# Optimization experiments

Hardware: AMD Instinct MI355X
Metric: run time of the kernel (lower is better)

## Reference

```python
import jax, jax.numpy as jnp
import numpy as np

N_NODES = 50000
N_EDGES = 800000
D_NODE = 128
D_EDGE = 64
N_GC = 2
H = 256
N_GRAPHS = 512


def setup_inputs() -> dict:
    key = jax.random.key(0)
    ks = jax.random.split(key, 32)
    s = 0.05
    inp = {
        'x': jax.random.normal(ks[0], (N_NODES, D_NODE), jnp.float32),
        'edge_index': jax.random.randint(ks[1], (2, N_EDGES), 0, N_NODES, jnp.int64 if jax.config.jax_enable_x64 else jnp.int32),
        'edge_attr': jax.random.normal(ks[2], (N_EDGES, D_EDGE), jnp.float32),
        'batch': jnp.sort(jax.random.randint(ks[3], (N_NODES,), 0, N_GRAPHS)),
    }
    zin = 2 * D_NODE + D_EDGE  # 320
    inp['conv_Wf'] = jax.random.normal(ks[4], (N_GC, D_NODE, zin), jnp.float32) * s
    inp['conv_bf'] = jnp.zeros((N_GC, D_NODE), jnp.float32)
    inp['conv_Ws'] = jax.random.normal(ks[5], (N_GC, D_NODE, zin), jnp.float32) * s
    inp['conv_bs'] = jnp.zeros((N_GC, D_NODE), jnp.float32)
    # mlp_1: Linear(128->256), ReLU, Linear(256->256), ReLU, proj Linear(256->128)
    inp['mlp1_W0'] = jax.random.normal(ks[6], (H, D_NODE), jnp.float32) * s
    inp['mlp1_b0'] = jnp.zeros((H,), jnp.float32)
    inp['mlp1_W1'] = jax.random.normal(ks[7], (H, H), jnp.float32) * s
    inp['mlp1_b1'] = jnp.zeros((H,), jnp.float32)
    inp['mlp1_Wp'] = jax.random.normal(ks[8], (D_NODE, H), jnp.float32) * s
    inp['mlp1_bp'] = jnp.zeros((D_NODE,), jnp.float32)
    # mlp_2: same structure
    inp['mlp2_W0'] = jax.random.normal(ks[9], (H, D_NODE), jnp.float32) * s
    inp['mlp2_b0'] = jnp.zeros((H,), jnp.float32)
    inp['mlp2_W1'] = jax.random.normal(ks[10], (H, H), jnp.float32) * s
    inp['mlp2_b1'] = jnp.zeros((H,), jnp.float32)
    inp['mlp2_Wp'] = jax.random.normal(ks[11], (D_NODE, H), jnp.float32) * s
    inp['mlp2_bp'] = jnp.zeros((D_NODE,), jnp.float32)
    inp['out_W'] = jax.random.normal(ks[12], (1, D_NODE), jnp.float32) * s
    inp['out_b'] = jnp.zeros((1,), jnp.float32)
    return inp


def _mlp(x, W0, b0, W1, b1, Wp, bp):
    h = jax.nn.relu(x @ W0.T + b0)
    h = jax.nn.relu(h @ W1.T + b1)
    return h @ Wp.T + bp


def _cgconv(x, src, dst, edge_attr, Wf, bf, Ws, bs):
    # z = [x_i (target), x_j (source), edge_attr]  -> [E, 2D+De]
    z = jnp.concatenate([x[dst], x[src], edge_attr], axis=-1)
    msg = jax.nn.sigmoid(z @ Wf.T + bf) * jax.nn.softplus(z @ Ws.T + bs)
    aggr = jax.ops.segment_sum(msg, dst, num_segments=x.shape[0])
    return x + aggr  # CGConv residual


def reference(x, edge_index, edge_attr, batch,
              conv_Wf, conv_bf, conv_Ws, conv_bs,
              mlp1_W0, mlp1_b0, mlp1_W1, mlp1_b1, mlp1_Wp, mlp1_bp,
              mlp2_W0, mlp2_b0, mlp2_W1, mlp2_b1, mlp2_Wp, mlp2_bp,
              out_W, out_b):
    src, dst = edge_index[0], edge_index[1]
    out = x
    for l in range(N_GC):
        out = _cgconv(out, src, dst, edge_attr, conv_Wf[l], conv_bf[l], conv_Ws[l], conv_bs[l])
    out = out + _mlp(out, mlp1_W0, mlp1_b0, mlp1_W1, mlp1_b1, mlp1_Wp, mlp1_bp)
    out = jax.ops.segment_sum(out, batch, num_segments=N_GRAPHS)  # global_add_pool
    out = out + _mlp(out, mlp2_W0, mlp2_b0, mlp2_W1, mlp2_b1, mlp2_Wp, mlp2_bp)
    out = out @ out_W.T + out_b  # [n_graphs, 1]
    return out
```

## Files before the change

### kernel.cpp

```cpp
#include <hip/hip_runtime.h>
#include <stdint.h>

#define NN 50000
#define NE 800000
#define DN 128
#define DE 64
#define NG 512
#define HD 256
#define LDA 72
#define SPK_S 132

typedef unsigned short ushort_t;
typedef __attribute__((ext_vector_type(8))) short short8;
typedef __attribute__((ext_vector_type(4))) float floatx4;

__device__ __forceinline__ float bflo(unsigned u){ unsigned v=u<<16; float f; __builtin_memcpy(&f,&v,4); return f; }
__device__ __forceinline__ float bfhi(unsigned u){ unsigned v=u&0xffff0000u; float f; __builtin_memcpy(&f,&v,4); return f; }
__device__ __forceinline__ ushort_t f2bf(float f){ unsigned u; __builtin_memcpy(&u,&f,4); u += 0x7FFFu + ((u>>16)&1u); return (ushort_t)(u>>16); }
__device__ __forceinline__ unsigned cvtpk(float a, float b){
#if __has_builtin(__builtin_amdgcn_cvt_pk_bf16_f32)
  auto r = __builtin_amdgcn_cvt_pk_bf16_f32(a,b);
  unsigned u; __builtin_memcpy(&u,&r,4); return u;
#else
  return (unsigned)f2bf(a) | ((unsigned)f2bf(b)<<16);
#endif
}

__device__ __forceinline__ float actv(float fv, float sv){
  const float L2E = 1.44269504f, LN2 = 0.69314718f;
  float ef  = __builtin_amdgcn_exp2f(-L2E*fv);
  float sig = __builtin_amdgcn_rcpf(1.f+ef);
  float t   = __builtin_amdgcn_exp2f(-L2E*fabsf(sv));
  float sp  = fmaxf(sv,0.f) + LN2*__builtin_amdgcn_logf(1.f+t);
  return sig*sp;
}

__global__ void k_prep(const float* __restrict__ Wf, const float* __restrict__ Ws,
                       const float* __restrict__ W0, const float* __restrict__ W1, const float* __restrict__ Wp,
                       const float* __restrict__ cbf, const float* __restrict__ cbs,
                       ushort_t* Wnode, ushort_t* Wedge, ushort_t* W0b, ushort_t* W1b, ushort_t* Wpb,
                       float* bias512){
  int i = blockIdx.x*256 + threadIdx.x;
  if(i < 131072){
    int l = i >> 16, r = i & 65535;
    int n = r >> 7, k = r & 127;
    const float* W = (n<256)? Wf : Ws;
    int nn = n & 127;
    int koff = ((n>>7)&1) ? 128+k : k;
    Wnode[i] = f2bf(W[(size_t)l*128*320 + (size_t)nn*320 + koff]);
  } else if(i < 163840){
    int j = i - 131072;
    int l = j >> 14, r = j & 16383;
    int n = r >> 6, k = r & 63;
    const float* W = (n<128)? Wf : Ws;
    int nn = n & 127;
    Wedge[j] = f2bf(W[(size_t)l*128*320 + (size_t)nn*320 + 256 + k]);
  } else if(i < 196608){
    int j = i - 163840; W0b[j] = f2bf(W0[j]);
  } else if(i < 262144){
    int j = i - 196608; W1b[j] = f2bf(W1[j]);
  } else if(i < 294912){
    int j = i - 262144; Wpb[j] = f2bf(Wp[j]);
  } else if(i < 295936){
    int j = i - 294912;
    int l = j >> 9, c = j & 511;
    float v = 0.f;
    if(c < 128) v = cbf[l*128 + c];
    else if(c >= 256 && c < 384) v = cbs[l*128 + (c-256)];
    bias512[j] = v;
  }
}

__global__ void k_init_x(const float* x, float* xcur, ushort_t* xb){
  int i = blockIdx.x*256 + threadIdx.x;
  if(i < NN*DN){ float v = x[i]; xcur[i]=v; xb[i]=f2bf(v); }
}

__global__ void k_zero_u32(unsigned* p, int n){
  int i = blockIdx.x*256 + threadIdx.x;
  if(i<n) p[i]=0u;
}

__global__ void k_hist(const int* dst, int* deg){
  int i = blockIdx.x*256 + threadIdx.x;
  if(i<NE) atomicAdd(&deg[dst[i]], 1);
}

__global__ void k_blocksum(const int* deg, int* bsum, int n){
  __shared__ int s[256];
  int t = threadIdx.x, i = blockIdx.x*256 + t;
  s[t] = (i<n)? deg[i] : 0;
  __syncthreads();
  for(int o=128;o>0;o>>=1){ if(t<o) s[t]+=s[t+o]; __syncthreads(); }
  if(t==0) bsum[blockIdx.x]=s[0];
}

__global__ void k_scan_bsum(int* bsum, int nb, int* offs, int nnodes){
  __shared__ int s[2][256];
  int t = threadIdx.x;
  int v = (t<nb)? bsum[t] : 0;
  s[0][t]=v; __syncthreads();
  int cur=0;
  for(int o=1;o<256;o<<=1){
    int nx=cur^1;
    s[nx][t] = s[cur][t] + ((t>=o)? s[cur][t-o] : 0);
    cur=nx; __syncthreads();
  }
  if(t<nb) bsum[t] = s[cur][t] - v;
  if(t==255) offs[nnodes] = s[cur][255];
}

__global__ void k_scanscatter(const int* deg, const int* bsum, int* offs, int* cursor, int n){
  __shared__ int s[2][256];
  int t=threadIdx.x, i=blockIdx.x*256+t;
  int v=(i<n)? deg[i] : 0;
  s[0][t]=v; __syncthreads();
  int cur=0;
  for(int o=1;o<256;o<<=1){
    int nx=cur^1;
    s[nx][t] = s[cur][t] + ((t>=o)? s[cur][t-o] : 0);
    cur=nx; __syncthreads();
  }
  if(i<n){ int ex = s[cur][t]-v + bsum[blockIdx.x]; offs[i]=ex; cursor[i]=ex; }
}

__global__ void k_scatter(const int* dst, int* cursor, int* csr_pos){
  int i = blockIdx.x*256 + threadIdx.x;
  if(i<NE){ int pos = atomicAdd(&cursor[dst[i]], 1); csr_pos[i]=pos; }
}

__global__ __launch_bounds__(256) void k_gemm(const ushort_t* __restrict__ Ain, const ushort_t* __restrict__ Wg,
      int M, int N, int K, const float* __restrict__ bias, int mode,
      ushort_t* __restrict__ outb, float* __restrict__ outf, const float* __restrict__ addf){
  __shared__ __align__(16) ushort_t As[64*LDA];
  __shared__ __align__(16) ushort_t Bs[64*LDA];
  int tid = threadIdx.x;
  int m0 = blockIdx.x*64, n0 = blockIdx.y*64;
  int w = tid>>6, lane = tid&63, row16 = lane&15, quad = lane>>4;
  floatx4 acc[4];
  #pragma unroll
  for(int t=0;t<4;t++) acc[t]=(floatx4)(0.f);
  int nk = K>>6;
  for(int kc=0; kc<nk; kc++){
    #pragma unroll
    for(int i=0;i<2;i++){
      int lin = tid + i*256;
      int row = lin>>3, c8 = (lin&7)*8;
      uint4 va;
      int gm = m0+row;
      if(gm < M) va = *(const uint4*)&Ain[(size_t)gm*K + kc*64 + c8];
      else va = make_uint4(0,0,0,0);
      *(uint4*)&As[row*LDA + c8] = va;
      uint4 vb = *(const uint4*)&Wg[(size_t)(n0+row)*K + kc*64 + c8];
      *(uint4*)&Bs[row*LDA + c8] = vb;
    }
    __syncthreads();
    #pragma unroll
    for(int ks=0;ks<2;ks++){
      short8 a = *(const short8*)&As[(w*16+row16)*LDA + ks*32 + quad*8];
      #pragma unroll
      for(int t=0;t<4;t++){
        short8 b = *(const short8*)&Bs[(t*16+row16)*LDA + ks*32 + quad*8];
        acc[t] = __builtin_amdgcn_mfma_f32_16x16x32_bf16(a,b,acc[t],0,0,0);
      }
    }
    __syncthreads();
  }
  #pragma unroll
  for(int t=0;t<4;t++){
    int nn = n0 + t*16 + row16;
    #pragma unroll
    for(int r=0;r<4;r++){
      int m = m0 + w*16 + quad*4 + r;
      if(m>=M) continue;
      float v = acc[t][r];
      if(bias) v += bias[nn];
      if(mode==1){ v = v>0.f? v:0.f; outb[(size_t)m*N+nn]=f2bf(v); }
      else if(mode==2){ v += addf[(size_t)m*N+nn]; outf[(size_t)m*N+nn]=v; }
      else { outb[(size_t)m*N+nn]=f2bf(v); }
    }
  }
}

__global__ __launch_bounds__(256) void k_edge_msg(const float* __restrict__ ea,
      const int* __restrict__ src_g, const int* __restrict__ dst_g,
      const int* __restrict__ csr_pos,
      const ushort_t* __restrict__ Wedge, const ushort_t* __restrict__ Atab,
      ushort_t* __restrict__ msg){
  __shared__ __align__(16) char smem[46848];
  ushort_t* We  = (ushort_t*)smem;
  unsigned* spk = (unsigned*)smem;
  ushort_t* el  = (ushort_t*)(smem + 36864);
  int*      dl  = (int*)(smem + 46080);
  int*      sl  = (int*)(smem + 46336);
  int*      cp  = (int*)(smem + 46592);

  int tid = threadIdx.x;
  int e0 = blockIdx.x*64;
  {
    const uint4* s = (const uint4*)Wedge;
    #pragma unroll
    for(int i=0;i<8;i++){
      int idx = tid + i*256;
      int row = idx>>3, col = (idx&7)*8;
      *(uint4*)&We[row*LDA + col] = s[idx];
    }
  }
  {
    int row = tid>>2, c0 = (tid&3)*16;
    const float4* p = (const float4*)&ea[(size_t)(e0+row)*64 + c0];
    float4 f0=p[0], f1=p[1], f2=p[2], f3=p[3];
    uint4 q0, q1;
    q0.x=cvtpk(f0.x,f0.y); q0.y=cvtpk(f0.z,f0.w); q0.z=cvtpk(f1.x,f1.y); q0.w=cvtpk(f1.z,f1.w);
    q1.x=cvtpk(f2.x,f2.y); q1.y=cvtpk(f2.z,f2.w); q1.z=cvtpk(f3.x,f3.y); q1.w=cvtpk(f3.z,f3.w);
    *(uint4*)&el[row*LDA + c0] = q0;
    *(uint4*)&el[row*LDA + c0 + 8] = q1;
  }
  if(tid<64){ dl[tid]=dst_g[e0+tid]; sl[tid]=src_g[e0+tid]; }
  else if(tid>=64 && tid<128){ cp[tid-64]=csr_pos[e0+tid-64]; }
  __syncthreads();

  int w = tid>>6, lane = tid&63, row16 = lane&15, quad = lane>>4;
  floatx4 acc[16];
  #pragma unroll
  for(int t=0;t<16;t++) acc[t]=(floatx4)(0.f);
  #pragma unroll
  for(int ks=0;ks<2;ks++){
    short8 a = *(const short8*)&el[(w*16+row16)*LDA + ks*32 + quad*8];
    #pragma unroll
    for(int t=0;t<16;t++){
      short8 b = *(const short8*)&We[(t*16+row16)*LDA + ks*32 + quad*8];
      acc[t]=__builtin_amdgcn_mfma_f32_16x16x32_bf16(a,b,acc[t],0,0,0);
    }
  }
  __syncthreads();

  #pragma unroll
  for(int t=0;t<8;t++){
    int c = t*16 + row16;
    #pragma unroll
    for(int r=0;r<4;r++){
      int rl = w*16 + quad*4 + r;
      spk[rl*SPK_S + c] = cvtpk(acc[t][r], acc[t+8][r]);
    }
  }
  __syncthreads();

  #pragma unroll
  for(int j=0;j<4;j++){
    int id  = j*256 + tid;
    int eli = id >> 4;
    int c0  = (id & 15) * 8;
    int d = dl[eli], s = sl[eli], mrow = cp[eli];
    const unsigned* base = &spk[eli*SPK_S + c0];
    uint4 q0 = *(const uint4*)(base);
    uint4 q1 = *(const uint4*)(base + 4);
    const ushort_t* Adp = Atab + (size_t)d*512;
    const ushort_t* Asp = Atab + (size_t)s*512;
    uint4 a0 = *(const uint4*)&Adp[c0];
    uint4 a1 = *(const uint4*)&Asp[128+c0];
    uint4 a2 = *(const uint4*)&Adp[256+c0];
    uint4 a3 = *(const uint4*)&Asp[384+c0];
    unsigned qs[8] = {q0.x,q0.y,q0.z,q0.w,q1.x,q1.y,q1.z,q1.w};
    unsigned A0[4] = {a0.x,a0.y,a0.z,a0.w};
    unsigned A1[4] = {a1.x,a1.y,a1.z,a1.w};
    unsigned A2[4] = {a2.x,a2.y,a2.z,a2.w};
    unsigned A3[4] = {a3.x,a3.y,a3.z,a3.w};
    unsigned outw[4];
    #pragma unroll
    for(int k=0;k<4;k++){
      float fv0 = bflo(qs[2*k])   + bflo(A0[k]) + bflo(A1[k]);
      float sv0 = bfhi(qs[2*k])   + bflo(A2[k]) + bflo(A3[k]);
      float fv1 = bflo(qs[2*k+1]) + bfhi(A0[k]) + bfhi(A1[k]);
      float sv1 = bfhi(qs[2*k+1]) + bfhi(A2[k]) + bfhi(A3[k]);
      outw[k] = cvtpk(actv(fv0,sv0), actv(fv1,sv1));
    }
    uint4 o4; o4.x=outw[0]; o4.y=outw[1]; o4.z=outw[2]; o4.w=outw[3];
    *(uint4*)&msg[(size_t)mrow*128 + c0] = o4;
  }
}

__global__ __launch_bounds__(256) void k_aggregate(const ushort_t* __restrict__ msg,
      const int* __restrict__ offs, float* __restrict__ xcur, ushort_t* __restrict__ xb){
  int v = blockIdx.x*4 + (threadIdx.x>>6);
  int lane = threadIdx.x & 63;
  int rslot = lane>>4;
  int c0 = (lane&15)*8;
  int b = offs[v], e = offs[v+1];
  float acc[8];
  #pragma unroll
  for(int k=0;k<8;k++) acc[k]=0.f;
  for(int r=b+rslot; r<e; r+=4){
    uint4 m = *(const uint4*)&msg[(size_t)r*128 + c0];
    acc[0]+=bflo(m.x); acc[1]+=bfhi(m.x);
    acc[2]+=bflo(m.y); acc[3]+=bfhi(m.y);
    acc[4]+=bflo(m.z); acc[5]+=bfhi(m.z);
    acc[6]+=bflo(m.w); acc[7]+=bfhi(m.w);
  }
  #pragma unroll
  for(int k=0;k<8;k++){
    acc[k] += __shfl_xor(acc[k],16);
    acc[k] += __shfl_xor(acc[k],32);
  }
  if(rslot==0){
    float4 x0 = *(float4*)&xcur[(size_t)v*128+c0];
    float4 x1 = *(float4*)&xcur[(size_t)v*128+c0+4];
    x0.x+=acc[0]; x0.y+=acc[1]; x0.z+=acc[2]; x0.w+=acc[3];
    x1.x+=acc[4]; x1.y+=acc[5]; x1.z+=acc[6]; x1.w+=acc[7];
    *(float4*)&xcur[(size_t)v*128+c0]=x0;
    *(float4*)&xcur[(size_t)v*128+c0+4]=x1;
    uint4 o; o.x=cvtpk(x0.x,x0.y); o.y=cvtpk(x0.z,x0.w); o.z=cvtpk(x1.x,x1.y); o.w=cvtpk(x1.z,x1.w);
    *(uint4*)&xb[(size_t)v*128+c0]=o;
  }
}

__global__ __launch_bounds__(256) void k_pool(const float* __restrict__ xcur,
      const int* __restrict__ batch, float* __restrict__ pooled){
  int b0 = blockIdx.x * 128;
  int ch = threadIdx.x & 127;
  int half = threadIdx.x >> 7;
  int n0 = b0 + half*64;
  if(n0 >= NN) return;
  int n1 = n0 + 64; if(n1 > NN) n1 = NN;
  float sum = 0.f;
  int bid = batch[n0];
  for(int n=n0; n<n1; n++){
    int b = batch[n];
    if(b != bid){ atomicAdd(&pooled[(size_t)bid*128+ch], sum); sum=0.f; bid=b; }
    sum += xcur[(size_t)n*128 + ch];
  }
  atomicAdd(&pooled[(size_t)bid*128+ch], sum);
}

__global__ __launch_bounds__(256) void k_final(const float* __restrict__ pooled,
   const float* __restrict__ W0, const float* __restrict__ b0,
   const float* __restrict__ W1, const float* __restrict__ b1,
   const float* __restrict__ Wp, const float* __restrict__ bp,
   const float* __restrict__ outW, const float* __restrict__ outB,
   float* __restrict__ out){
  __shared__ float p[128], h0[256], h1[256], red[256];
  int g = blockIdx.x, t = threadIdx.x;
  if(t<128) p[t]=pooled[(size_t)g*128+t];
  __syncthreads();
  {
    const float4* wr = (const float4*)&W0[(size_t)t*128];
    float s=0.f;
    #pragma unroll 8
    for(int k=0;k<32;k++){ float4 wv=wr[k]; s += wv.x*p[k*4]+wv.y*p[k*4+1]+wv.z*p[k*4+2]+wv.w*p[k*4+3]; }
    s += b0[t]; h0[t] = s>0.f? s:0.f;
  }
  __syncthreads();
  {
    const float4* wr = (const float4*)&W1[(size_t)t*256];
    float s=0.f;
    #pragma unroll 8
    for(int k=0;k<64;k++){ float4 wv=wr[k]; s += wv.x*h0[k*4]+wv.y*h0[k*4+1]+wv.z*h0[k*4+2]+wv.w*h0[k*4+3]; }
    s += b1[t]; h1[t] = s>0.f? s:0.f;
  }
  __syncthreads();
  float rt = 0.f;
  if(t<128){
    const float4* wr=(const float4*)&Wp[(size_t)t*256];
    float s=0.f;
    #pragma unroll 8
    for(int k=0;k<64;k++){ float4 wv=wr[k]; s += wv.x*h1[k*4]+wv.y*h1[k*4+1]+wv.z*h1[k*4+2]+wv.w*h1[k*4+3]; }
    s += bp[t] + p[t];
    rt = s * outW[t];
  }
  red[t]=rt; __syncthreads();
  for(int o=128;o>0;o>>=1){ if(t<o) red[t]+=red[t+o]; __syncthreads(); }
  if(t==0) out[g] = red[0] + outB[0];
}

extern "C" void kernel_launch(void* const* d_in, const int* in_sizes, int n_in,
                              void* d_out, int out_size, void* d_ws, size_t ws_size,
                              hipStream_t stream){
  const float* x    = (const float*)d_in[0];
  const int*   ei   = (const int*)d_in[1];
  const float* ea   = (const float*)d_in[2];
  const int*   batch= (const int*)d_in[3];
  const float* cWf  = (const float*)d_in[4];
  const float* cbf  = (const float*)d_in[5];
  const float* cWs  = (const float*)d_in[6];
  const float* cbs  = (const float*)d_in[7];
  const float* W0   = (const float*)d_in[8];
  const float* b0   = (const float*)d_in[9];
  const float* W1   = (const float*)d_in[10];
  const float* b1   = (const float*)d_in[11];
  const float* Wp   = (const float*)d_in[12];
  const float* bp   = (const float*)d_in[13];
  const float* m2W0 = (const float*)d_in[14];
  const float* m2b0 = (const float*)d_in[15];
  const float* m2W1 = (const float*)d_in[16];
  const float* m2b1 = (const float*)d_in[17];
  const float* m2Wp = (const float*)d_in[18];
  const float* m2bp = (const float*)d_in[19];
  const float* outW = (const float*)d_in[20];
  const float* outB = (const float*)d_in[21];

  const int* srcp = ei;
  const int* dstp = ei + NE;

  char* ws = (char*)d_ws;
  size_t off = 0;
  auto alloc = [&](size_t bytes)->char*{
    char* p = ws + off;
    off += (bytes + 255) & ~(size_t)255;
    return p;
  };
  float*    xcur   = (float*)   alloc((size_t)NN*DN*4);
  ushort_t* xb     = (ushort_t*)alloc((size_t)NN*DN*2);
  ushort_t* Atab   = (ushort_t*)alloc((size_t)NN*512*2);
  ushort_t* msg    = (ushort_t*)alloc((size_t)NE*128*2);
  ushort_t* Wnode  = (ushort_t*)alloc((size_t)2*512*128*2);
  ushort_t* Wedge  = (ushort_t*)alloc((size_t)2*256*64*2);
  ushort_t* W0b    = (ushort_t*)alloc((size_t)256*128*2);
  ushort_t* W1b    = (ushort_t*)alloc((size_t)256*256*2);
  ushort_t* Wpb    = (ushort_t*)alloc((size_t)128*256*2);
  float*    bias512= (float*)   alloc((size_t)2*512*4);
  int*      deg    = (int*)     alloc((size_t)NN*4);
  int*      offs   = (int*)     alloc((size_t)(NN+1)*4);
  int*      cursor = (int*)     alloc((size_t)NN*4);
  int*      csr_pos= (int*)     alloc((size_t)NE*4);
  int*      bsum   = (int*)     alloc(256*4);
  float*    pooled = (float*)   alloc((size_t)NG*DN*4);
  ushort_t* h0 = Atab;
  ushort_t* h1 = Atab + (size_t)NN*256;

  k_prep<<<1156, 256, 0, stream>>>(cWf, cWs, W0, W1, Wp, cbf, cbs,
                                   Wnode, Wedge, W0b, W1b, Wpb, bias512);
  k_init_x<<<(NN*DN+255)/256, 256, 0, stream>>>(x, xcur, xb);

  int nb = (NN+255)/256;
  k_zero_u32<<<(NN+255)/256, 256, 0, stream>>>((unsigned*)deg, NN);
  k_hist<<<(NE+255)/256, 256, 0, stream>>>(dstp, deg);
  k_blocksum<<<nb, 256, 0, stream>>>(deg, bsum, NN);
  k_scan_bsum<<<1, 256, 0, stream>>>(bsum, nb, offs, NN);
  k_scanscatter<<<nb, 256, 0, stream>>>(deg, bsum, offs, cursor, NN);
  k_scatter<<<(NE+255)/256, 256, 0, stream>>>(dstp, cursor, csr_pos);

  for(int l=0;l<2;l++){
    dim3 ga((NN+63)/64, 512/64);
    k_gemm<<<ga, 256, 0, stream>>>(xb, Wnode + (size_t)l*512*128, NN, 512, 128,
                                   bias512 + l*512, 0, Atab, nullptr, nullptr);
    k_edge_msg<<<NE/64, 256, 0, stream>>>(ea, srcp, dstp, csr_pos,
                                          Wedge + (size_t)l*256*64, Atab, msg);
    k_aggregate<<<NN/4, 256, 0, stream>>>(msg, offs, xcur, xb);
  }

  {
    dim3 g0((NN+63)/64, 256/64);
    k_gemm<<<g0, 256, 0, stream>>>(xb, W0b, NN, 256, 128, b0, 1, h0, nullptr, nullptr);
    dim3 g1((NN+63)/64, 256/64);
    k_gemm<<<g1, 256, 0, stream>>>(h0, W1b, NN, 256, 256, b1, 1, h1, nullptr, nullptr);
    dim3 g2((NN+63)/64, 128/64);
    k_gemm<<<g2, 256, 0, stream>>>(h1, Wpb, NN, 128, 256, bp, 2, nullptr, xcur, xcur);
  }

  k_zero_u32<<<(NG*DN+255)/256, 256, 0, stream>>>((unsigned*)pooled, NG*DN);
  k_pool<<<(NN+127)/128, 256, 0, stream>>>(xcur, batch, pooled);

  k_final<<<NG, 256, 0, stream>>>(pooled, m2W0, m2b0, m2W1, m2b1, m2Wp, m2bp,
                                  outW, outB, (float*)d_out);
  (void)in_sizes; (void)n_in; (void)out_size; (void)ws_size;
}
```

Measured before the change: 1.015 ms.

## Pre-permute edge data into CSR order and swizzle edge-message shared memory

Adds a permutation pass that converts edge attributes to bf16 once and stores them, together with src/dst indices, in CSR (dst-sorted) order. Both edge-message layers can then read contiguous bf16 rows and write msg sequentially instead of scattering through csr_pos. It also replaces padded LDS rows with an XOR swizzle, shrinks shared memory, changes the SPK stride, and folds the degree zeroing into the prep kernel. The cost is an extra permutation kernel plus more workspace; the Atab gathers become dst-sorted, which should improve locality.

Result: slower. 1.090 ms (+7.4%).

```diff
diff --git a/kernel.cpp b/kernel.cpp
--- a/kernel.cpp
+++ b/kernel.cpp
@@ -8,7 +8,7 @@
 #define NG 512
 #define HD 256
 #define LDA 72
-#define SPK_S 132
+#define SPK_S 130
 
 typedef unsigned short ushort_t;
 typedef __attribute__((ext_vector_type(8))) short short8;
@@ -39,7 +39,7 @@
                        const float* __restrict__ W0, const float* __restrict__ W1, const float* __restrict__ Wp,
                        const float* __restrict__ cbf, const float* __restrict__ cbs,
                        ushort_t* Wnode, ushort_t* Wedge, ushort_t* W0b, ushort_t* W1b, ushort_t* Wpb,
-                       float* bias512){
+                       float* bias512, int* deg){
   int i = blockIdx.x*256 + threadIdx.x;
   if(i < 131072){
     int l = i >> 16, r = i & 65535;
@@ -68,6 +68,8 @@
     if(c < 128) v = cbf[l*128 + c];
     else if(c >= 256 && c < 384) v = cbs[l*128 + (c-256)];
     bias512[j] = v;
+  } else if(i < 295936 + NN){
+    deg[i - 295936] = 0;
   }
 }
 
@@ -129,6 +131,23 @@
   if(i<NE){ int pos = atomicAdd(&cursor[dst[i]], 1); csr_pos[i]=pos; }
 }
 
+__global__ __launch_bounds__(256) void k_permute(const float* __restrict__ ea,
+      const int* __restrict__ src_g, const int* __restrict__ dst_g,
+      const int* __restrict__ csr_pos,
+      ushort_t* __restrict__ eab, int* __restrict__ src_csr, int* __restrict__ dst_csr){
+  int id = blockIdx.x*256 + threadIdx.x;
+  if(id >= NE*8) return;
+  int e = id>>3, seg = id&7;
+  int pos = csr_pos[e];
+  const float4* p = (const float4*)&ea[(size_t)e*64 + seg*8];
+  float4 f0 = p[0], f1 = p[1];
+  uint4 q;
+  q.x = cvtpk(f0.x,f0.y); q.y = cvtpk(f0.z,f0.w);
+  q.z = cvtpk(f1.x,f1.y); q.w = cvtpk(f1.z,f1.w);
+  *(uint4*)&eab[(size_t)pos*64 + seg*8] = q;
+  if(seg==0){ src_csr[pos] = src_g[e]; dst_csr[pos] = dst_g[e]; }
+}
+
 __global__ __launch_bounds__(256) void k_gemm(const ushort_t* __restrict__ Ain, const ushort_t* __restrict__ Wg,
       int M, int N, int K, const float* __restrict__ bias, int mode,
       ushort_t* __restrict__ outb, float* __restrict__ outf, const float* __restrict__ addf){
@@ -182,18 +201,14 @@
   }
 }
 
-__global__ __launch_bounds__(256) void k_edge_msg(const float* __restrict__ ea,
-      const int* __restrict__ src_g, const int* __restrict__ dst_g,
-      const int* __restrict__ csr_pos,
+__global__ __launch_bounds__(256) void k_edge_msg(const ushort_t* __restrict__ eab_g,
+      const int* __restrict__ src_csr, const int* __restrict__ dst_csr,
       const ushort_t* __restrict__ Wedge, const ushort_t* __restrict__ Atab,
       ushort_t* __restrict__ msg){
-  __shared__ __align__(16) char smem[46848];
+  __shared__ __align__(16) char smem[40960];
   ushort_t* We  = (ushort_t*)smem;
   unsigned* spk = (unsigned*)smem;
-  ushort_t* el  = (ushort_t*)(smem + 36864);
-  int*      dl  = (int*)(smem + 46080);
-  int*      sl  = (int*)(smem + 46336);
-  int*      cp  = (int*)(smem + 46592);
+  ushort_t* el  = (ushort_t*)(smem + 32768);
 
   int tid = threadIdx.x;
   int e0 = blockIdx.x*64;
@@ -201,23 +216,22 @@
     const uint4* s = (const uint4*)Wedge;
     #pragma unroll
     for(int i=0;i<8;i++){
-      int idx = tid + i*256;
-      int row = idx>>3, col = (idx&7)*8;
-      *(uint4*)&We[row*LDA + col] = s[idx];
+      int g = tid + i*256;
+      int row = g>>3, ch = g&7;
+      int pch = ch ^ (row&7);
+      *(uint4*)&We[row*64 + pch*8] = s[g];
     }
   }
   {
-    int row = tid>>2, c0 = (tid&3)*16;
-    const float4* p = (const float4*)&ea[(size_t)(e0+row)*64 + c0];
-    float4 f0=p[0], f1=p[1], f2=p[2], f3=p[3];
-    uint4 q0, q1;
-    q0.x=cvtpk(f0.x,f0.y); q0.y=cvtpk(f0.z,f0.w); q0.z=cvtpk(f1.x,f1.y); q0.w=cvtpk(f1.z,f1.w);
-    q1.x=cvtpk(f2.x,f2.y); q1.y=cvtpk(f2.z,f2.w); q1.z=cvtpk(f3.x,f3.y); q1.w=cvtpk(f3.z,f3.w);
-    *(uint4*)&el[row*LDA + c0] = q0;
-    *(uint4*)&el[row*LDA + c0 + 8] = q1;
-  }
-  if(tid<64){ dl[tid]=dst_g[e0+tid]; sl[tid]=src_g[e0+tid]; }
-  else if(tid>=64 && tid<128){ cp[tid-64]=csr_pos[e0+tid-64]; }
+    const uint4* s = (const uint4*)eab_g + (size_t)e0*8;
+    #pragma unroll
+    for(int i=0;i<2;i++){
+      int g = tid + i*256;
+      int row = g>>3, ch = g&7;
+      int pch = ch ^ (row&7);
+      *(uint4*)&el[row*64 + pch*8] = s[g];
+    }
+  }
   __syncthreads();
 
   int w = tid>>6, lane = tid&63, row16 = lane&15, quad = lane>>4;
@@ -226,10 +240,11 @@
   for(int t=0;t<16;t++) acc[t]=(floatx4)(0.f);
   #pragma unroll
   for(int ks=0;ks<2;ks++){
-    short8 a = *(const short8*)&el[(w*16+row16)*LDA + ks*32 + quad*8];
+    int pch = (ks*4+quad) ^ (row16&7);
+    short8 a = *(const short8*)&el[(w*16+row16)*64 + pch*8];
     #pragma unroll
     for(int t=0;t<16;t++){
-      short8 b = *(const short8*)&We[(t*16+row16)*LDA + ks*32 + quad*8];
+      short8 b = *(const short8*)&We[(t*16+row16)*64 + pch*8];
       acc[t]=__builtin_amdgcn_mfma_f32_16x16x32_bf16(a,b,acc[t],0,0,0);
     }
   }
@@ -251,7 +266,8 @@
     int id  = j*256 + tid;
     int eli = id >> 4;
     int c0  = (id & 15) * 8;
-    int d = dl[eli], s = sl[eli], mrow = cp[eli];
+    int e   = e0 + eli;
+    int d = dst_csr[e], s = src_csr[e];
     const unsigned* base = &spk[eli*SPK_S + c0];
     uint4 q0 = *(const uint4*)(base);
     uint4 q1 = *(const uint4*)(base + 4);
@@ -276,7 +292,7 @@
       outw[k] = cvtpk(actv(fv0,sv0), actv(fv1,sv1));
     }
     uint4 o4; o4.x=outw[0]; o4.y=outw[1]; o4.z=outw[2]; o4.w=outw[3];
-    *(uint4*)&msg[(size_t)mrow*128 + c0] = o4;
+    *(uint4*)&msg[(size_t)e*128 + c0] = o4;
   }
 }
 
@@ -412,6 +428,7 @@
   ushort_t* xb     = (ushort_t*)alloc((size_t)NN*DN*2);
   ushort_t* Atab   = (ushort_t*)alloc((size_t)NN*512*2);
   ushort_t* msg    = (ushort_t*)alloc((size_t)NE*128*2);
+  ushort_t* eab    = (ushort_t*)alloc((size_t)NE*64*2);
   ushort_t* Wnode  = (ushort_t*)alloc((size_t)2*512*128*2);
   ushort_t* Wedge  = (ushort_t*)alloc((size_t)2*256*64*2);
   ushort_t* W0b    = (ushort_t*)alloc((size_t)256*128*2);
@@ -422,28 +439,30 @@
   int*      offs   = (int*)     alloc((size_t)(NN+1)*4);
   int*      cursor = (int*)     alloc((size_t)NN*4);
   int*      csr_pos= (int*)     alloc((size_t)NE*4);
+  int*      src_csr= (int*)     alloc((size_t)NE*4);
+  int*      dst_csr= (int*)     alloc((size_t)NE*4);
   int*      bsum   = (int*)     alloc(256*4);
   float*    pooled = (float*)   alloc((size_t)NG*DN*4);
   ushort_t* h0 = Atab;
   ushort_t* h1 = Atab + (size_t)NN*256;
 
-  k_prep<<<1156, 256, 0, stream>>>(cWf, cWs, W0, W1, Wp, cbf, cbs,
-                                   Wnode, Wedge, W0b, W1b, Wpb, bias512);
+  k_prep<<<(295936+NN+255)/256, 256, 0, stream>>>(cWf, cWs, W0, W1, Wp, cbf, cbs,
+                                   Wnode, Wedge, W0b, W1b, Wpb, bias512, deg);
   k_init_x<<<(NN*DN+255)/256, 256, 0, stream>>>(x, xcur, xb);
 
   int nb = (NN+255)/256;
-  k_zero_u32<<<(NN+255)/256, 256, 0, stream>>>((unsigned*)deg, NN);
   k_hist<<<(NE+255)/256, 256, 0, stream>>>(dstp, deg);
   k_blocksum<<<nb, 256, 0, stream>>>(deg, bsum, NN);
   k_scan_bsum<<<1, 256, 0, stream>>>(bsum, nb, offs, NN);
   k_scanscatter<<<nb, 256, 0, stream>>>(deg, bsum, offs, cursor, NN);
   k_scatter<<<(NE+255)/256, 256, 0, stream>>>(dstp, cursor, csr_pos);
+  k_permute<<<(NE*8+255)/256, 256, 0, stream>>>(ea, srcp, dstp, csr_pos, eab, src_csr, dst_csr);
 
   for(int l=0;l<2;l++){
     dim3 ga((NN+63)/64, 512/64);
     k_gemm<<<ga, 256, 0, stream>>>(xb, Wnode + (size_t)l*512*128, NN, 512, 128,
                                    bias512 + l*512, 0, Atab, nullptr, nullptr);
-    k_edge_msg<<<NE/64, 256, 0, stream>>>(ea, srcp, dstp, csr_pos,
+    k_edge_msg<<<NE/64, 256, 0, stream>>>(eab, src_csr, dst_csr,
                                           Wedge + (size_t)l*256*64, Atab, msg);
     k_aggregate<<<NN/4, 256, 0, stream>>>(msg, offs, xcur, xb);
   }
```
